# Optimization experiments

Measured on AMD Instinct MI355X. Metric: run time of the kernel, lower is better.

Reference implementation:

```python
import jax, jax.numpy as jnp
import numpy as np

N = 100_000      # nodes
E = 1_600_000    # edges (avg degree 16)
C_IN = 128
HID = 128        # 2 * out_channels
OUT = 64
EDIM = 1
NEG_SLOPE = 0.2  # PyG GATConv default negative_slope


def _gat(x, src, dst, n, W, a_s, a_d, b, edge_attr=None, We=None, a_e=None):
    """PyG GATConv with heads=1, concat=True, add_self_loops=True (fill_value='mean').
    x: [n, Cin]; src/dst: [E] (messages flow src -> dst); returns [n, Cout].
    """
    xl = x @ W                 # [n, Cout] transformed node features
    a_src = xl @ a_s           # [n] per-node source attention logit
    a_dst = xl @ a_d           # [n] per-node destination attention logit
    loop = jnp.arange(n)
    if edge_attr is not None:
        # self-loop edge_attr = mean of incoming edge_attr per node (fill_value='mean')
        ones = jnp.ones((src.shape[0],), xl.dtype)
        cnt = jax.ops.segment_sum(ones, dst, num_segments=n)              # [n]
        s = jax.ops.segment_sum(edge_attr, dst, num_segments=n)           # [n, EDIM]
        loop_attr = jnp.where(cnt[:, None] > 0, s / jnp.maximum(cnt, 1.0)[:, None], 0.0)
        ea = jnp.concatenate([edge_attr, loop_attr], axis=0)              # [E+n, EDIM]
    src2 = jnp.concatenate([src, loop])
    dst2 = jnp.concatenate([dst, loop])
    alpha = a_src[src2] + a_dst[dst2]                                      # [E+n]
    if edge_attr is not None:
        alpha = alpha + (ea @ We) @ a_e                                    # edge-attribute attention term
    alpha = jax.nn.leaky_relu(alpha, NEG_SLOPE)
    # softmax over incoming edges of each destination node (stable)
    m = jax.ops.segment_max(alpha, dst2, num_segments=n)
    ex = jnp.exp(alpha - m[dst2])
    den = jax.ops.segment_sum(ex, dst2, num_segments=n)
    coef = ex / den[dst2]                                                  # [E+n]
    out = jax.ops.segment_sum(coef[:, None] * xl[src2], dst2, num_segments=n)
    return out + b


def setup_inputs() -> dict:
    key = jax.random.key(0)
    ks = jax.random.split(key, 32)
    s = 0.1
    inp = {
        "x": jax.random.normal(ks[0], (N, C_IN), jnp.float32),
        "edge_index": jax.random.randint(ks[1], (2, E), 0, N, jnp.int64),
        "edge_weights": jax.random.uniform(ks[2], (E, EDIM), jnp.float32),
    }
    def lin(k, i, o):
        return jax.random.normal(k, (i, o), jnp.float32) * s
    def vec(k, c):
        return jax.random.normal(k, (c,), jnp.float32) * s
    # layer 0: 128 -> 128 (with edge attention)
    inp["W0"], inp["as0"], inp["ad0"] = lin(ks[3], C_IN, HID), vec(ks[4], HID), vec(ks[5], HID)
    inp["ae0"], inp["We0"], inp["b0"] = vec(ks[6], HID), lin(ks[7], EDIM, HID), jnp.zeros((HID,), jnp.float32)
    # layer 1: 128 -> 128 (with edge attention)
    inp["W1"], inp["as1"], inp["ad1"] = lin(ks[8], HID, HID), vec(ks[9], HID), vec(ks[10], HID)
    inp["ae1"], inp["We1"], inp["b1"] = vec(ks[11], HID), lin(ks[12], EDIM, HID), jnp.zeros((HID,), jnp.float32)
    # conv_mu: 128 -> 64 (with edge attention)
    inp["Wm"], inp["asm"], inp["adm"] = lin(ks[13], HID, OUT), vec(ks[14], OUT), vec(ks[15], OUT)
    inp["aem"], inp["Wem"], inp["bm"] = vec(ks[16], OUT), lin(ks[17], EDIM, OUT), jnp.zeros((OUT,), jnp.float32)
    # conv_logstd: 128 -> 64 (called WITHOUT edge_attr -> no edge term)
    inp["Wl"], inp["asl"], inp["adl"] = lin(ks[18], HID, OUT), vec(ks[19], OUT), vec(ks[20], OUT)
    inp["bl"] = jnp.zeros((OUT,), jnp.float32)
    return inp


def reference(x, edge_index, edge_weights,
              W0, as0, ad0, ae0, We0, b0,
              W1, as1, ad1, ae1, We1, b1,
              Wm, asm, adm, aem, Wem, bm,
              Wl, asl, adl, bl):
    src, dst = edge_index[0], edge_index[1]
    h = jax.nn.relu(_gat(x, src, dst, N, W0, as0, ad0, b0, edge_weights, We0, ae0))
    h = jax.nn.relu(_gat(h, src, dst, N, W1, as1, ad1, b1, edge_weights, We1, ae1))
    mu = _gat(h, src, dst, N, Wm, asm, adm, bm, edge_weights, Wem, aem)
    logstd = _gat(h, src, dst, N, Wl, asl, adl, bl)  # no edge_attr, per original forward
    return mu, logstd
```

## Files before the change

### kernel.cpp

```cpp
#include <hip/hip_runtime.h>

#define NN 100000
#define EE 1600000
#define NBK 782
#define NBKP 784
#define NBLK 391
#define NBLKP 392
#define SETB 207

typedef __attribute__((ext_vector_type(8))) __bf16 bf16x8;
typedef __attribute__((ext_vector_type(4))) float f32x4;
typedef unsigned short u16;

__device__ __forceinline__ float bf2f(u16 v) {
  union { unsigned u; float f; } x; x.u = ((unsigned)v) << 16; return x.f;
}
__device__ __forceinline__ u16 f2bf(float f) {
  union { unsigned u; float f; } x; x.f = f;
  x.u += 0x7fffu + ((x.u >> 16) & 1u);
  return (u16)(x.u >> 16);
}
__device__ __forceinline__ float lo_f(unsigned u) {
  union { unsigned u; float f; } x; x.u = u << 16; return x.f;
}
__device__ __forceinline__ float hi_f(unsigned u) {
  union { unsigned u; float f; } x; x.u = u & 0xffff0000u; return x.f;
}
__device__ __forceinline__ unsigned pack2(float a, float b) {
  return (unsigned)f2bf(a) | ((unsigned)f2bf(b) << 16);
}
__device__ __forceinline__ float lrelu(float x) { return x > 0.f ? x : 0.2f * x; }
__device__ __forceinline__ int clampi(int v, int hi) {
  return ((unsigned)v < (unsigned)hi) ? v : 0;
}
__device__ __forceinline__ float ldf(const void* p, size_t i, int fl) {
  return fl ? ((const float*)p)[i] : bf2f(((const u16*)p)[i]);
}

__device__ __forceinline__ int wave_fdetect(const u16* __restrict__ xb) {
  int lane = threadIdx.x & 63;
  int bad = 0;
#pragma unroll
  for (int j = 0; j < 4; ++j) {
    float a = fabsf(bf2f(xb[lane * 4 + j]));
    bad |= (!(a == a) || a > 1e6f) ? 1 : 0;
  }
  return (__ballot(bad) != 0ull) ? 1 : 0;
}
__device__ __forceinline__ int wave_mdetect(const int* __restrict__ ei) {
  int lane = threadIdx.x & 63;
  int v = (lane < 32) ? ei[2 * lane + 1] : 0;
  return (__ballot(v != 0) == 0ull) ? 1 : 0;
}

__global__ void k_fillf(float* __restrict__ o, int n, float v) {
  int i = blockIdx.x * 256 + threadIdx.x;
  if (i < n) o[i] = v;
}

struct CvtDesc { const void* src; u16* dst; int n; };
struct SetupArgs {
  CvtDesc cvt[12];
  const void* W[4]; u16* WT[4]; int WM[4];
  const void* dw[3]; const void* da[3]; int dm[3];
  float* cvals;
  const u16* xb;
  const int* ei;
  int* histM;
};
__global__ __launch_bounds__(256) void k_setup(SetupArgs a) {
  __shared__ int h[NBKP];
  int b = blockIdx.x, t = threadIdx.x;
  if (b >= SETB) {
    int blk = b - SETB;
    int m_ = wave_mdetect(a.ei);
    for (int j = t; j < NBKP; j += 256) h[j] = 0;
    __syncthreads();
#pragma unroll
    for (int j = 0; j < 16; ++j) {
      int e = blk * 4096 + j * 256 + t;
      if (e < EE) {
        int d = m_ ? a.ei[2 * (size_t)(EE + e)] : a.ei[EE + e];
        d = clampi(d, NN);
        atomicAdd(&h[d >> 7], 1);
      }
    }
    __syncthreads();
    for (int j = t; j < NBKP; j += 256) a.histM[j * NBLKP + blk] = h[j];
    return;
  }
  if (b < 12) {
    int fl = wave_fdetect(a.xb);
    const void* src = a.cvt[b].src; u16* dst = a.cvt[b].dst; int n = a.cvt[b].n;
    for (int i = t; i < n; i += 256)
      dst[i] = fl ? f2bf(((const float*)src)[i]) : ((const u16*)src)[i];
    return;
  }
  b -= 12;
  if (b < 192) {
    int fl = wave_fdetect(a.xb);
    int wsel, lb;
    if (b < 64)       { wsel = 0; lb = b; }
    else if (b < 128) { wsel = 1; lb = b - 64; }
    else if (b < 160) { wsel = 2; lb = b - 128; }
    else              { wsel = 3; lb = b - 160; }
    int M = a.WM[wsel];
    int i = lb * 256 + t;
    if (i < 128 * M) {
      int k = i / M, m = i % M;
      a.WT[wsel][m * 128 + k] = f2bf(ldf(a.W[wsel], i, fl));
    }
    return;
  }
  b -= 192;
  if (b < 3) {
    if (t < 64) {
      int fl = wave_fdetect(a.xb);
      float s = 0.f; int m = a.dm[b];
      for (int j = t; j < m; j += 64) s += ldf(a.dw[b], j, fl) * ldf(a.da[b], j, fl);
      for (int off = 32; off; off >>= 1) s += __shfl_xor(s, off);
      if (t == 0) a.cvals[b] = s;
    }
    return;
  }
}

__global__ __launch_bounds__(512) void k_scanA(int* __restrict__ histM,
                                               int* __restrict__ binTot) {
  int b = blockIdx.x, t = threadIdx.x;
  int v = (t < NBLK) ? histM[b * NBLKP + t] : 0;
  int lane = t & 63, w = t >> 6;
  int sc = v;
  for (int off = 1; off < 64; off <<= 1) {
    int o = __shfl_up(sc, off); if (lane >= off) sc += o;
  }
  __shared__ int wt[8];
  if (lane == 63) wt[w] = sc;
  __syncthreads();
  int add = 0;
  for (int k = 0; k < w; ++k) add += wt[k];
  int excl = sc - v + add;
  if (t < NBLK) histM[b * NBLKP + t] = excl;
  if (t == 511) binTot[b] = excl;
}

__global__ __launch_bounds__(256) void k_scanB(const int* __restrict__ binTot,
                                               int* __restrict__ bucketBase,
                                               int* __restrict__ row_off) {
  int t = threadIdx.x;
  int v[4]; int s = 0;
#pragma unroll
  for (int j = 0; j < 4; ++j) {
    int idx = t * 4 + j;
    v[j] = (idx < NBK) ? binTot[idx] : 0;
    s += v[j];
  }
  int lane = t & 63, w = t >> 6;
  int sc = s;
  for (int off = 1; off < 64; off <<= 1) {
    int o = __shfl_up(sc, off); if (lane >= off) sc += o;
  }
  __shared__ int wt[4];
  if (lane == 63) wt[w] = sc;
  __syncthreads();
  int add = 0;
  for (int k = 0; k < w; ++k) add += wt[k];
  int ex = add + sc - s;
#pragma unroll
  for (int j = 0; j < 4; ++j) {
    int idx = t * 4 + j;
    if (idx <= NBK) bucketBase[idx] = ex;
    ex += v[j];
  }
  if (t == 0) row_off[NN] = EE;
}

template<bool DUAL>
__device__ __forceinline__ void gemm_body(
    int bid, int fl, const void* __restrict__ Araw,
    const u16* __restrict__ WT,
    const u16* __restrict__ avs, const u16* __restrict__ avd,
    u16* __restrict__ xl,
    float* __restrict__ asrc, float* __restrict__ adst,
    float2* __restrict__ asAB, float* __restrict__ adstB, int n) {
  const int K = 128;
  int lane = threadIdx.x & 63;
  int wave = threadIdx.x >> 6;
  int quad = lane >> 4;
  int l16 = lane & 15;
  int r0 = (bid * 4 + wave) * 16;
  if (r0 >= n) return;
  int arow = r0 + l16; if (arow >= n) arow = n - 1;
  bf16x8 afr[4];
  if (fl) {
    const float* af = (const float*)Araw + (size_t)arow * K + quad * 8;
#pragma unroll
    for (int kb = 0; kb < 4; ++kb) {
      float4 f0 = *(const float4*)(af + kb * 32);
      float4 f1 = *(const float4*)(af + kb * 32 + 4);
      union { bf16x8 v; u16 s[8]; } t;
      t.s[0] = f2bf(f0.x); t.s[1] = f2bf(f0.y); t.s[2] = f2bf(f0.z); t.s[3] = f2bf(f0.w);
      t.s[4] = f2bf(f1.x); t.s[5] = f2bf(f1.y); t.s[6] = f2bf(f1.z); t.s[7] = f2bf(f1.w);
      afr[kb] = t.v;
    }
  } else {
    const u16* ab = (const u16*)Araw + (size_t)arow * K + quad * 8;
#pragma unroll
    for (int kb = 0; kb < 4; ++kb) afr[kb] = *(const bf16x8*)(ab + kb * 32);
  }
  f32x4 acc[8];
#pragma unroll
  for (int nb = 0; nb < 8; ++nb) acc[nb] = (f32x4){0.f, 0.f, 0.f, 0.f};
#pragma unroll
  for (int nb = 0; nb < 8; ++nb) {
    const u16* bbase = WT + (size_t)(nb * 16 + l16) * K + quad * 8;
#pragma unroll
    for (int kb = 0; kb < 4; ++kb) {
      bf16x8 bfr = *(const bf16x8*)(bbase + kb * 32);
      acc[nb] = __builtin_amdgcn_mfma_f32_16x16x32_bf16(afr[kb], bfr, acc[nb], 0, 0, 0);
    }
  }
  float ps[2][4] = {{0,0,0,0},{0,0,0,0}}, pd[2][4] = {{0,0,0,0},{0,0,0,0}};
#pragma unroll
  for (int nb = 0; nb < 8; ++nb) {
    const int g = (DUAL && nb >= 4) ? 1 : 0;
    int col = nb * 16 + l16;
    float vs = bf2f(avs[col]), vd = bf2f(avd[col]);
#pragma unroll
    for (int r = 0; r < 4; ++r) {
      int row = r0 + quad * 4 + r;
      float v = acc[nb][r];
      if (row < n) xl[(size_t)row * 128 + col] = f2bf(v);
      ps[g][r] += v * vs;
      pd[g][r] += v * vd;
    }
  }
#pragma unroll
  for (int off = 1; off < 16; off <<= 1) {
#pragma unroll
    for (int r = 0; r < 4; ++r) {
      ps[0][r] += __shfl_xor(ps[0][r], off);
      pd[0][r] += __shfl_xor(pd[0][r], off);
      if (DUAL) {
        ps[1][r] += __shfl_xor(ps[1][r], off);
        pd[1][r] += __shfl_xor(pd[1][r], off);
      }
    }
  }
  if (l16 == 0) {
#pragma unroll
    for (int r = 0; r < 4; ++r) {
      int row = r0 + quad * 4 + r;
      if (row < n) {
        if (DUAL) {
          asAB[row] = make_float2(ps[0][r], ps[1][r]);
          adst[row] = pd[0][r]; adstB[row] = pd[1][r];
        } else {
          asrc[row] = ps[0][r]; adst[row] = pd[0][r];
        }
      }
    }
  }
}

__global__ __launch_bounds__(256) void k_esgemm(
    const int* __restrict__ ei, const void* __restrict__ ew,
    const u16* __restrict__ xb, const int* __restrict__ histM,
    const int* __restrict__ bucketBase, int2* __restrict__ stage,
    const void* __restrict__ Araw, const u16* __restrict__ WT,
    const u16* __restrict__ avs, const u16* __restrict__ avd,
    u16* __restrict__ xl, float* __restrict__ asrc, float* __restrict__ adst, int n) {
  __shared__ int lbase[NBKP];
  __shared__ int cur[NBKP];
  if ((int)blockIdx.x >= NBLK) {
    int fl = wave_fdetect(xb);
    gemm_body<false>((int)blockIdx.x - NBLK, fl, Araw, WT, avs, avd,
                     xl, asrc, adst, nullptr, nullptr, n);
    return;
  }
  int blk = blockIdx.x, t = threadIdx.x;
  int m_ = wave_mdetect(ei);
  int fl = wave_fdetect(xb);
  for (int j = t; j < NBKP; j += 256) {
    int bb = (j < NBK) ? (bucketBase[j] + histM[j * NBLKP + blk]) : 0;
    lbase[j] = bb; cur[j] = 0;
  }
  __syncthreads();
#pragma unroll
  for (int j = 0; j < 16; ++j) {
    int e = blk * 4096 + j * 256 + t;
    if (e < EE) {
      int s = m_ ? ei[2 * (size_t)e] : ei[e];
      int d = m_ ? ei[2 * (size_t)(EE + e)] : ei[EE + e];
      s = clampi(s, NN);
      d = clampi(d, NN);
      int bin = d >> 7, low = d & 127;
      int r = atomicAdd(&cur[bin], 1);
      int pos = lbase[bin] + r;
      if (pos >= 0 && pos < EE)
        stage[pos] = make_int2(s, (low << 16) | (int)f2bf(ldf(ew, e, fl)));
    }
  }
}

__global__ __launch_bounds__(256) void k_bucket(
    const int2* __restrict__ stage, const int* __restrict__ bucketBase,
    int2* __restrict__ edges, int* __restrict__ row_off, float* __restrict__ la) {
  __shared__ int hist[128];
  __shared__ float wsum[128];
  __shared__ int pref[128];
  __shared__ int cur[128];
  int b = blockIdx.x, t = threadIdx.x;
  int base = bucketBase[b], n = bucketBase[b + 1] - base;
  if (t < 128) { hist[t] = 0; wsum[t] = 0.f; cur[t] = 0; }
  __syncthreads();
  for (int i = t; i < n; i += 256) {
    int2 it = stage[base + i];
    int bin = (it.y >> 16) & 127;
    atomicAdd(&hist[bin], 1);
    atomicAdd(&wsum[bin], bf2f((u16)(it.y & 0xffff)));
  }
  __syncthreads();
  if (t == 0) {
    int run = 0;
    for (int j = 0; j < 128; ++j) { pref[j] = run; run += hist[j]; }
  }
  __syncthreads();
  if (t < 128) {
    int d = b * 128 + t;
    if (d < NN) {
      row_off[d] = base + pref[t];
      la[d] = hist[t] ? wsum[t] / (float)hist[t] : 0.f;
    }
  }
  for (int i = t; i < n; i += 256) {
    int2 it = stage[base + i];
    int bin = (it.y >> 16) & 127;
    int r = atomicAdd(&cur[bin], 1);
    edges[base + pref[bin] + r] = it;
  }
}

template<bool DUAL>
__global__ __launch_bounds__(256) void k_gemm(
    const u16* __restrict__ A, const u16* __restrict__ WT,
    const u16* __restrict__ avs, const u16* __restrict__ avd,
    u16* __restrict__ xl, float* __restrict__ asrc, float* __restrict__ adst,
    float2* __restrict__ asAB, float* __restrict__ adstB, int n) {
  gemm_body<DUAL>(blockIdx.x, 0, A, WT, avs, avd, xl, asrc, adst, asAB, adstB, n);
}

__global__ __launch_bounds__(256) void k_agg(
    const int* __restrict__ row_off, const int2* __restrict__ edges,
    const float* __restrict__ asrc, const float* __restrict__ adst,
    const float* __restrict__ la, const float* __restrict__ cptr,
    const u16* __restrict__ xl, const u16* __restrict__ bias,
    u16* __restrict__ out, int n) {
  __shared__ float lp[16][16];
  __shared__ int lsv[16][16];
  int tid = blockIdx.x * 256 + threadIdx.x;
  int d = tid >> 4;
  if (d >= n) return;
  int l = threadIdx.x & 15;
  int grp = threadIdx.x >> 4;
  float c = cptr[0];
  float ad = adst[d];
  float aL = lrelu(asrc[d] + ad + c * la[d]);
  float lsum = 0.f;
  int4 su = *(const int4*)(xl + (size_t)d * 128 + l * 8);
  float A0 = lo_f(su.x), A1 = hi_f(su.x), A2 = lo_f(su.y), A3 = hi_f(su.y);
  float A4 = lo_f(su.z), A5 = hi_f(su.z), A6 = lo_f(su.w), A7 = hi_f(su.w);
  float B0 = 0.f, B1 = 0.f, B2 = 0.f, B3 = 0.f, B4 = 0.f, B5 = 0.f, B6 = 0.f, B7 = 0.f;
  int beg = row_off[d], end = row_off[d + 1];
  for (int base = beg; base < end; base += 16) {
    int i = base + l;
    bool v = i < end;
    int2 ev = v ? edges[i] : make_int2(0, 0);
    float e = 0.f;
    if (v) e = __expf(lrelu(asrc[ev.x] + ad + c * bf2f((u16)(ev.y & 0xffff))) - aL);
    lsum += e;
    lp[grp][l] = e; lsv[grp][l] = ev.x;
    int cnt = end - base; if (cnt > 16) cnt = 16;
    int j = 0;
    for (; j + 4 <= cnt; j += 4) {
      float p0 = lp[grp][j + 0]; int s0 = lsv[grp][j + 0];
      float p1 = lp[grp][j + 1]; int s1 = lsv[grp][j + 1];
      float p2 = lp[grp][j + 2]; int s2 = lsv[grp][j + 2];
      float p3 = lp[grp][j + 3]; int s3 = lsv[grp][j + 3];
      int4 u0 = *(const int4*)(xl + (size_t)s0 * 128 + l * 8);
      int4 u1 = *(const int4*)(xl + (size_t)s1 * 128 + l * 8);
      int4 u2 = *(const int4*)(xl + (size_t)s2 * 128 + l * 8);
      int4 u3 = *(const int4*)(xl + (size_t)s3 * 128 + l * 8);
      A0 = fmaf(p0, lo_f(u0.x), A0); A1 = fmaf(p0, hi_f(u0.x), A1);
      A2 = fmaf(p0, lo_f(u0.y), A2); A3 = fmaf(p0, hi_f(u0.y), A3);
      A4 = fmaf(p0, lo_f(u0.z), A4); A5 = fmaf(p0, hi_f(u0.z), A5);
      A6 = fmaf(p0, lo_f(u0.w), A6); A7 = fmaf(p0, hi_f(u0.w), A7);
      B0 = fmaf(p1, lo_f(u1.x), B0); B1 = fmaf(p1, hi_f(u1.x), B1);
      B2 = fmaf(p1, lo_f(u1.y), B2); B3 = fmaf(p1, hi_f(u1.y), B3);
      B4 = fmaf(p1, lo_f(u1.z), B4); B5 = fmaf(p1, hi_f(u1.z), B5);
      B6 = fmaf(p1, lo_f(u1.w), B6); B7 = fmaf(p1, hi_f(u1.w), B7);
      A0 = fmaf(p2, lo_f(u2.x), A0); A1 = fmaf(p2, hi_f(u2.x), A1);
      A2 = fmaf(p2, lo_f(u2.y), A2); A3 = fmaf(p2, hi_f(u2.y), A3);
      A4 = fmaf(p2, lo_f(u2.z), A4); A5 = fmaf(p2, hi_f(u2.z), A5);
      A6 = fmaf(p2, lo_f(u2.w), A6); A7 = fmaf(p2, hi_f(u2.w), A7);
      B0 = fmaf(p3, lo_f(u3.x), B0); B1 = fmaf(p3, hi_f(u3.x), B1);
      B2 = fmaf(p3, lo_f(u3.y), B2); B3 = fmaf(p3, hi_f(u3.y), B3);
      B4 = fmaf(p3, lo_f(u3.z), B4); B5 = fmaf(p3, hi_f(u3.z), B5);
      B6 = fmaf(p3, lo_f(u3.w), B6); B7 = fmaf(p3, hi_f(u3.w), B7);
    }
    for (; j + 2 <= cnt; j += 2) {
      float p0 = lp[grp][j];     int s0 = lsv[grp][j];
      float p1 = lp[grp][j + 1]; int s1 = lsv[grp][j + 1];
      int4 u0 = *(const int4*)(xl + (size_t)s0 * 128 + l * 8);
      int4 u1 = *(const int4*)(xl + (size_t)s1 * 128 + l * 8);
      A0 = fmaf(p0, lo_f(u0.x), A0); A1 = fmaf(p0, hi_f(u0.x), A1);
      A2 = fmaf(p0, lo_f(u0.y), A2); A3 = fmaf(p0, hi_f(u0.y), A3);
      A4 = fmaf(p0, lo_f(u0.z), A4); A5 = fmaf(p0, hi_f(u0.z), A5);
      A6 = fmaf(p0, lo_f(u0.w), A6); A7 = fmaf(p0, hi_f(u0.w), A7);
      B0 = fmaf(p1, lo_f(u1.x), B0); B1 = fmaf(p1, hi_f(u1.x), B1);
      B2 = fmaf(p1, lo_f(u1.y), B2); B3 = fmaf(p1, hi_f(u1.y), B3);
      B4 = fmaf(p1, lo_f(u1.z), B4); B5 = fmaf(p1, hi_f(u1.z), B5);
      B6 = fmaf(p1, lo_f(u1.w), B6); B7 = fmaf(p1, hi_f(u1.w), B7);
    }
    if (j < cnt) {
      float p0 = lp[grp][j]; int s0 = lsv[grp][j];
      int4 u0 = *(const int4*)(xl + (size_t)s0 * 128 + l * 8);
      A0 = fmaf(p0, lo_f(u0.x), A0); A1 = fmaf(p0, hi_f(u0.x), A1);
      A2 = fmaf(p0, lo_f(u0.y), A2); A3 = fmaf(p0, hi_f(u0.y), A3);
      A4 = fmaf(p0, lo_f(u0.z), A4); A5 = fmaf(p0, hi_f(u0.z), A5);
      A6 = fmaf(p0, lo_f(u0.w), A6); A7 = fmaf(p0, hi_f(u0.w), A7);
    }
  }
  A0 += B0; A1 += B1; A2 += B2; A3 += B3; A4 += B4; A5 += B5; A6 += B6; A7 += B7;
#pragma unroll
  for (int off = 1; off < 16; off <<= 1) lsum += __shfl_xor(lsum, off);
  float inv = 1.f / (lsum + 1.f);
  int4 bv = *(const int4*)(bias + l * 8);
  float o0 = fmaxf(fmaf(A0, inv, lo_f((unsigned)bv.x)), 0.f);
  float o1 = fmaxf(fmaf(A1, inv, hi_f((unsigned)bv.x)), 0.f);
  float o2 = fmaxf(fmaf(A2, inv, lo_f((unsigned)bv.y)), 0.f);
  float o3 = fmaxf(fmaf(A3, inv, hi_f((unsigned)bv.y)), 0.f);
  float o4 = fmaxf(fmaf(A4, inv, lo_f((unsigned)bv.z)), 0.f);
  float o5 = fmaxf(fmaf(A5, inv, hi_f((unsigned)bv.z)), 0.f);
  float o6 = fmaxf(fmaf(A6, inv, lo_f((unsigned)bv.w)), 0.f);
  float o7 = fmaxf(fmaf(A7, inv, hi_f((unsigned)bv.w)), 0.f);
  int4 ov;
  ov.x = (int)pack2(o0, o1); ov.y = (int)pack2(o2, o3);
  ov.z = (int)pack2(o4, o5); ov.w = (int)pack2(o6, o7);
  *(int4*)(out + (size_t)d * 128 + l * 8) = ov;
}

__global__ __launch_bounds__(256) void k_aggh(
    const int* __restrict__ row_off, const int2* __restrict__ edges,
    const float2* __restrict__ asAB, const float* __restrict__ adA,
    const float* __restrict__ adB,
    const float* __restrict__ la, const float* __restrict__ cptr,
    const u16* __restrict__ xl, const u16* __restrict__ bias,
    float* __restrict__ outf, int n) {
  __shared__ float lpA[16][16];
  __shared__ float lpB[16][16];
  __shared__ int lsv[16][16];
  int tid = blockIdx.x * 256 + threadIdx.x;
  int d = tid >> 4;
  if (d >= n) return;
  int l = threadIdx.x & 15;
  int grp = threadIdx.x >> 4;
  bool isMu = l < 8;
  float c = cptr[0];
  float adAd = adA[d], adBd = adB[d];
  float2 abd = asAB[d];
  float aLA = lrelu(abd.x + adAd + c * la[d]);
  float aLB = lrelu(abd.y + adBd);
  float lsA = 0.f, lsB = 0.f;
  int4 su = *(const int4*)(xl + (size_t)d * 128 + l * 8);
  float A0 = lo_f(su.x), A1 = hi_f(su.x), A2 = lo_f(su.y), A3 = hi_f(su.y);
  float A4 = lo_f(su.z), A5 = hi_f(su.z), A6 = lo_f(su.w), A7 = hi_f(su.w);
  float B0 = 0.f, B1 = 0.f, B2 = 0.f, B3 = 0.f, B4 = 0.f, B5 = 0.f, B6 = 0.f, B7 = 0.f;
  int beg = row_off[d], end = row_off[d + 1];
  for (int base = beg; base < end; base += 16) {
    int i = base + l;
    bool v = i < end;
    int2 ev = v ? edges[i] : make_int2(0, 0);
    float eA = 0.f, eB = 0.f;
    if (v) {
      float2 ab = asAB[ev.x];
      eA = __expf(lrelu(ab.x + adAd + c * bf2f((u16)(ev.y & 0xffff))) - aLA);
      eB = __expf(lrelu(ab.y + adBd) - aLB);
    }
    lsA += eA; lsB += eB;
    lpA[grp][l] = eA; lpB[grp][l] = eB; lsv[grp][l] = ev.x;
    const float* lpp = isMu ? lpA[grp] : lpB[grp];
    int cnt = end - base; if (cnt > 16) cnt = 16;
    int j = 0;
    for (; j + 4 <= cnt; j += 4) {
      float p0 = lpp[j + 0]; int s0 = lsv[grp][j + 0];
      float p1 = lpp[j + 1]; int s1 = lsv[grp][j + 1];
      float p2 = lpp[j + 2]; int s2 = lsv[grp][j + 2];
      float p3 = lpp[j + 3]; int s3 = lsv[grp][j + 3];
      int4 u0 = *(const int4*)(xl + (size_t)s0 * 128 + l * 8);
      int4 u1 = *(const int4*)(xl + (size_t)s1 * 128 + l * 8);
      int4 u2 = *(const int4*)(xl + (size_t)s2 * 128 + l * 8);
      int4 u3 = *(const int4*)(xl + (size_t)s3 * 128 + l * 8);
      A0 = fmaf(p0, lo_f(u0.x), A0); A1 = fmaf(p0, hi_f(u0.x), A1);
      A2 = fmaf(p0, lo_f(u0.y), A2); A3 = fmaf(p0, hi_f(u0.y), A3);
      A4 = fmaf(p0, lo_f(u0.z), A4); A5 = fmaf(p0, hi_f(u0.z), A5);
      A6 = fmaf(p0, lo_f(u0.w), A6); A7 = fmaf(p0, hi_f(u0.w), A7);
      B0 = fmaf(p1, lo_f(u1.x), B0); B1 = fmaf(p1, hi_f(u1.x), B1);
      B2 = fmaf(p1, lo_f(u1.y), B2); B3 = fmaf(p1, hi_f(u1.y), B3);
      B4 = fmaf(p1, lo_f(u1.z), B4); B5 = fmaf(p1, hi_f(u1.z), B5);
      B6 = fmaf(p1, lo_f(u1.w), B6); B7 = fmaf(p1, hi_f(u1.w), B7);
      A0 = fmaf(p2, lo_f(u2.x), A0); A1 = fmaf(p2, hi_f(u2.x), A1);
      A2 = fmaf(p2, lo_f(u2.y), A2); A3 = fmaf(p2, hi_f(u2.y), A3);
      A4 = fmaf(p2, lo_f(u2.z), A4); A5 = fmaf(p2, hi_f(u2.z), A5);
      A6 = fmaf(p2, lo_f(u2.w), A6); A7 = fmaf(p2, hi_f(u2.w), A7);
      B0 = fmaf(p3, lo_f(u3.x), B0); B1 = fmaf(p3, hi_f(u3.x), B1);
      B2 = fmaf(p3, lo_f(u3.y), B2); B3 = fmaf(p3, hi_f(u3.y), B3);
      B4 = fmaf(p3, lo_f(u3.z), B4); B5 = fmaf(p3, hi_f(u3.z), B5);
      B6 = fmaf(p3, lo_f(u3.w), B6); B7 = fmaf(p3, hi_f(u3.w), B7);
    }
    for (; j + 2 <= cnt; j += 2) {
      float p0 = lpp[j];     int s0 = lsv[grp][j];
      float p1 = lpp[j + 1]; int s1 = lsv[grp][j + 1];
      int4 u0 = *(const int4*)(xl + (size_t)s0 * 128 + l * 8);
      int4 u1 = *(const int4*)(xl + (size_t)s1 * 128 + l * 8);
      A0 = fmaf(p0, lo_f(u0.x), A0); A1 = fmaf(p0, hi_f(u0.x), A1);
      A2 = fmaf(p0, lo_f(u0.y), A2); A3 = fmaf(p0, hi_f(u0.y), A3);
      A4 = fmaf(p0, lo_f(u0.z), A4); A5 = fmaf(p0, hi_f(u0.z), A5);
      A6 = fmaf(p0, lo_f(u0.w), A6); A7 = fmaf(p0, hi_f(u0.w), A7);
      B0 = fmaf(p1, lo_f(u1.x), B0); B1 = fmaf(p1, hi_f(u1.x), B1);
      B2 = fmaf(p1, lo_f(u1.y), B2); B3 = fmaf(p1, hi_f(u1.y), B3);
      B4 = fmaf(p1, lo_f(u1.z), B4); B5 = fmaf(p1, hi_f(u1.z), B5);
      B6 = fmaf(p1, lo_f(u1.w), B6); B7 = fmaf(p1, hi_f(u1.w), B7);
    }
    if (j < cnt) {
      float p0 = lpp[j]; int s0 = lsv[grp][j];
      int4 u0 = *(const int4*)(xl + (size_t)s0 * 128 + l * 8);
      A0 = fmaf(p0, lo_f(u0.x), A0); A1 = fmaf(p0, hi_f(u0.x), A1);
      A2 = fmaf(p0, lo_f(u0.y), A2); A3 = fmaf(p0, hi_f(u0.y), A3);
      A4 = fmaf(p0, lo_f(u0.z), A4); A5 = fmaf(p0, hi_f(u0.z), A5);
      A6 = fmaf(p0, lo_f(u0.w), A6); A7 = fmaf(p0, hi_f(u0.w), A7);
    }
  }
  A0 += B0; A1 += B1; A2 += B2; A3 += B3; A4 += B4; A5 += B5; A6 += B6; A7 += B7;
#pragma unroll
  for (int off = 1; off < 16; off <<= 1) {
    lsA += __shfl_xor(lsA, off);
    lsB += __shfl_xor(lsB, off);
  }
  float inv = 1.f / ((isMu ? lsA : lsB) + 1.f);
  int4 bv = *(const int4*)(bias + l * 8);
  float4 oa, ob;
  oa.x = fmaf(A0, inv, lo_f((unsigned)bv.x));
  oa.y = fmaf(A1, inv, hi_f((unsigned)bv.x));
  oa.z = fmaf(A2, inv, lo_f((unsigned)bv.y));
  oa.w = fmaf(A3, inv, hi_f((unsigned)bv.y));
  ob.x = fmaf(A4, inv, lo_f((unsigned)bv.z));
  ob.y = fmaf(A5, inv, hi_f((unsigned)bv.z));
  ob.z = fmaf(A6, inv, lo_f((unsigned)bv.w));
  ob.w = fmaf(A7, inv, hi_f((unsigned)bv.w));
  float* obase = isMu ? (outf + (size_t)d * 64 + l * 8)
                      : (outf + (size_t)NN * 64 + (size_t)d * 64 + (l - 8) * 8);
  *(float4*)obase = oa;
  *(float4*)(obase + 4) = ob;
}

extern "C" void kernel_launch(void* const* d_in, const int* in_sizes, int n_in,
                              void* d_out, int out_size, void* d_ws, size_t ws_size,
                              hipStream_t stream) {
  (void)in_sizes; (void)n_in;
  const int* ei = (const int*)d_in[1];
  const u16* xb = (const u16*)d_in[0];
  float* outf = (float*)d_out;

  u16* regionA = (u16*)d_out;
  u16* regionB = (u16*)d_out + (size_t)NN * 128;
  int* histM = (int*)d_out;
  int2* stage = (int2*)((char*)d_out + (size_t)2 * 1024 * 1024);

  char* p = (char*)d_ws;
  auto alloc = [&](size_t bytes) -> char* {
    char* r = p; p += (bytes + 255) & ~(size_t)255; return r;
  };
  int*   row_off   = (int*)alloc((NN + 1) * 4);
  int*   binTot    = (int*)alloc(NBKP * 4);
  int*   bucketBase= (int*)alloc((NBKP + 2) * 4);
  float* la        = (float*)alloc(NN * 4);
  float* asrcA     = (float*)alloc(NN * 4);
  float* adstA     = (float*)alloc(NN * 4);
  float* adstB     = (float*)alloc(NN * 4);
  float2* asAB     = (float2*)alloc((size_t)NN * 8);
  int2*  edges     = (int2*)alloc((size_t)EE * 8);
  u16*   WT0       = (u16*)alloc(128 * 128 * 2);
  u16*   WT1       = (u16*)alloc(128 * 128 * 2);
  u16*   WTh       = (u16*)alloc(128 * 128 * 2);
  float* cvals     = (float*)alloc(16);
  u16*   vecc      = (u16*)alloc(9 * 256);
  u16*   xl        = (u16*)alloc((size_t)NN * 128 * 2);

  size_t NEED = (size_t)(p - (char*)d_ws);
  if (ws_size < NEED) {
    k_fillf<<<(out_size + 255) / 256, 256, 0, stream>>>(outf, out_size, 0.125f);
    return;
  }

  u16* as0c = vecc + 0 * 128; u16* ad0c = vecc + 1 * 128; u16* b0c = vecc + 2 * 128;
  u16* as1c = vecc + 3 * 128; u16* ad1c = vecc + 4 * 128; u16* b1c = vecc + 5 * 128;
  u16* hvs  = vecc + 6 * 128; u16* hvd  = vecc + 7 * 128; u16* bh  = vecc + 8 * 128;

  SetupArgs sa;
  sa.cvt[0]  = {d_in[4],  as0c, 128};
  sa.cvt[1]  = {d_in[5],  ad0c, 128};
  sa.cvt[2]  = {d_in[8],  b0c,  128};
  sa.cvt[3]  = {d_in[10], as1c, 128};
  sa.cvt[4]  = {d_in[11], ad1c, 128};
  sa.cvt[5]  = {d_in[14], b1c,  128};
  sa.cvt[6]  = {d_in[16], hvs,      64};
  sa.cvt[7]  = {d_in[22], hvs + 64, 64};
  sa.cvt[8]  = {d_in[17], hvd,      64};
  sa.cvt[9]  = {d_in[23], hvd + 64, 64};
  sa.cvt[10] = {d_in[20], bh,       64};
  sa.cvt[11] = {d_in[24], bh + 64,  64};
  sa.W[0] = d_in[3];  sa.WT[0] = WT0;            sa.WM[0] = 128;
  sa.W[1] = d_in[9];  sa.WT[1] = WT1;            sa.WM[1] = 128;
  sa.W[2] = d_in[15]; sa.WT[2] = WTh;            sa.WM[2] = 64;
  sa.W[3] = d_in[21]; sa.WT[3] = WTh + 64 * 128; sa.WM[3] = 64;
  sa.dw[0] = d_in[7];  sa.da[0] = d_in[6];  sa.dm[0] = 128;
  sa.dw[1] = d_in[13]; sa.da[1] = d_in[12]; sa.dm[1] = 128;
  sa.dw[2] = d_in[19]; sa.da[2] = d_in[18]; sa.dm[2] = 64;
  sa.cvals = cvals; sa.xb = xb; sa.ei = ei; sa.histM = histM;
  k_setup<<<SETB + NBLK, 256, 0, stream>>>(sa);

  const int gblocks = (((NN + 15) / 16) + 3) / 4;
  const int eblocks16 = (int)(((size_t)NN * 16 + 255) / 256);

  k_scanA<<<NBK, 512, 0, stream>>>(histM, binTot);
  k_scanB<<<1, 256, 0, stream>>>(binTot, bucketBase, row_off);
  k_esgemm<<<NBLK + gblocks, 256, 0, stream>>>(ei, d_in[2], xb, histM, bucketBase,
                                               stage, d_in[0], WT0, as0c, ad0c,
                                               xl, asrcA, adstA, NN);
  k_bucket<<<NBK, 256, 0, stream>>>(stage, bucketBase, edges, row_off, la);

  k_agg<<<eblocks16, 256, 0, stream>>>(row_off, edges, asrcA, adstA, la,
                                       cvals + 0, xl, b0c, regionB, NN);
  k_gemm<false><<<gblocks, 256, 0, stream>>>(regionB, WT1, as1c, ad1c,
                                             xl, asrcA, adstA, nullptr, nullptr, NN);
  k_agg<<<eblocks16, 256, 0, stream>>>(row_off, edges, asrcA, adstA, la,
                                       cvals + 1, xl, b1c, regionA, NN);
  k_gemm<true><<<gblocks, 256, 0, stream>>>(regionA, WTh, hvs, hvd,
                                            xl, nullptr, adstA, asAB, adstB, NN);
  k_aggh<<<eblocks16, 256, 0, stream>>>(row_off, edges, asAB, adstA, adstB,
                                        la, cvals + 2, xl, bh, outf, NN);
}
```

Measured before the change: 515.2 us.

## Sort destination nodes by in-degree so aggregation waves get balanced work

New measurement: 535.7 us. +4.0%, slower.

```diff
diff --git a/kernel.cpp b/kernel.cpp
--- a/kernel.cpp
+++ b/kernel.cpp
@@ -269,16 +269,17 @@
     const int* __restrict__ bucketBase, int2* __restrict__ stage,
     const void* __restrict__ Araw, const u16* __restrict__ WT,
     const u16* __restrict__ avs, const u16* __restrict__ avd,
-    u16* __restrict__ xl, float* __restrict__ asrc, float* __restrict__ adst, int n) {
+    u16* __restrict__ xl, float* __restrict__ asrc, float* __restrict__ adst,
+    int n, int gemmBlocks) {
   __shared__ int lbase[NBKP];
   __shared__ int cur[NBKP];
-  if ((int)blockIdx.x >= NBLK) {
+  if ((int)blockIdx.x < gemmBlocks) {
     int fl = wave_fdetect(xb);
-    gemm_body<false>((int)blockIdx.x - NBLK, fl, Araw, WT, avs, avd,
+    gemm_body<false>(blockIdx.x, fl, Araw, WT, avs, avd,
                      xl, asrc, adst, nullptr, nullptr, n);
     return;
   }
-  int blk = blockIdx.x, t = threadIdx.x;
+  int blk = (int)blockIdx.x - gemmBlocks, t = threadIdx.x;
   int m_ = wave_mdetect(ei);
   int fl = wave_fdetect(xb);
   for (int j = t; j < NBKP; j += 256) {
@@ -305,14 +306,17 @@
 
 __global__ __launch_bounds__(256) void k_bucket(
     const int2* __restrict__ stage, const int* __restrict__ bucketBase,
-    int2* __restrict__ edges, int* __restrict__ row_off, float* __restrict__ la) {
+    int2* __restrict__ edges, int* __restrict__ row_off, float* __restrict__ la,
+    int* __restrict__ degM) {
   __shared__ int hist[128];
   __shared__ float wsum[128];
   __shared__ int pref[128];
   __shared__ int cur[128];
+  __shared__ int dh[32];
   int b = blockIdx.x, t = threadIdx.x;
   int base = bucketBase[b], n = bucketBase[b + 1] - base;
   if (t < 128) { hist[t] = 0; wsum[t] = 0.f; cur[t] = 0; }
+  if (t >= 128 && t < 160) dh[t - 128] = 0;
   __syncthreads();
   for (int i = t; i < n; i += 256) {
     int2 it = stage[base + i];
@@ -331,13 +335,72 @@
     if (d < NN) {
       row_off[d] = base + pref[t];
       la[d] = hist[t] ? wsum[t] / (float)hist[t] : 0.f;
-    }
-  }
+      int bin = hist[t] < 32 ? hist[t] : 31;
+      atomicAdd(&dh[bin], 1);
+    }
+  }
+  __syncthreads();
+  if (t < 32) degM[t * NBKP + b] = dh[t];
   for (int i = t; i < n; i += 256) {
     int2 it = stage[base + i];
     int bin = (it.y >> 16) & 127;
     int r = atomicAdd(&cur[bin], 1);
     edges[base + pref[bin] + r] = it;
+  }
+}
+
+__global__ __launch_bounds__(512) void k_scanD(int* __restrict__ degM,
+                                               int* __restrict__ binTotD) {
+  __shared__ int wt[8];
+  __shared__ int carrySh;
+  int b = blockIdx.x, t = threadIdx.x;
+  if (t == 0) carrySh = 0;
+  __syncthreads();
+  for (int half = 0; half < 2; ++half) {
+    int col = half * 512 + t;
+    int v = (col < NBK) ? degM[b * NBKP + col] : 0;
+    int lane = t & 63, w = t >> 6;
+    int sc = v;
+    for (int off = 1; off < 64; off <<= 1) {
+      int o = __shfl_up(sc, off); if (lane >= off) sc += o;
+    }
+    if (lane == 63) wt[w] = sc;
+    __syncthreads();
+    int add = 0;
+    for (int k = 0; k < w; ++k) add += wt[k];
+    int excl = carrySh + add + sc - v;
+    if (col < NBK) degM[b * NBKP + col] = excl;
+    __syncthreads();
+    if (t == 511) carrySh = excl + v;
+    __syncthreads();
+  }
+  if (t == 0) binTotD[b] = carrySh;
+}
+
+__global__ void k_scanE(const int* __restrict__ binTotD, int* __restrict__ binBaseD) {
+  int t = threadIdx.x;
+  int v = (t < 32) ? binTotD[t] : 0;
+  int sc = v;
+  for (int off = 1; off < 64; off <<= 1) {
+    int o = __shfl_up(sc, off); if (t >= off) sc += o;
+  }
+  if (t < 32) binBaseD[t] = sc - v;
+}
+
+__global__ __launch_bounds__(128) void k_dscatter(
+    const int* __restrict__ row_off, const int* __restrict__ degM,
+    const int* __restrict__ binBaseD, int* __restrict__ perm) {
+  __shared__ int cur[32];
+  int b = blockIdx.x, t = threadIdx.x;
+  if (t < 32) cur[t] = 0;
+  __syncthreads();
+  int d = b * 128 + t;
+  if (d < NN) {
+    int deg = row_off[d + 1] - row_off[d];
+    int bin = deg < 32 ? deg : 31;
+    int r = atomicAdd(&cur[bin], 1);
+    int pos = binBaseD[bin] + degM[bin * NBKP + b] + r;
+    if (pos >= 0 && pos < NN) perm[pos] = d;
   }
 }
 
@@ -351,6 +414,7 @@
 }
 
 __global__ __launch_bounds__(256) void k_agg(
+    const int* __restrict__ perm,
     const int* __restrict__ row_off, const int2* __restrict__ edges,
     const float* __restrict__ asrc, const float* __restrict__ adst,
     const float* __restrict__ la, const float* __restrict__ cptr,
@@ -359,8 +423,9 @@
   __shared__ float lp[16][16];
   __shared__ int lsv[16][16];
   int tid = blockIdx.x * 256 + threadIdx.x;
-  int d = tid >> 4;
-  if (d >= n) return;
+  int wid = tid >> 4;
+  if (wid >= n) return;
+  int d = perm[wid];
   int l = threadIdx.x & 15;
   int grp = threadIdx.x >> 4;
   float c = cptr[0];
@@ -451,6 +516,7 @@
 }
 
 __global__ __launch_bounds__(256) void k_aggh(
+    const int* __restrict__ perm,
     const int* __restrict__ row_off, const int2* __restrict__ edges,
     const float2* __restrict__ asAB, const float* __restrict__ adA,
     const float* __restrict__ adB,
@@ -461,8 +527,9 @@
   __shared__ float lpB[16][16];
   __shared__ int lsv[16][16];
   int tid = blockIdx.x * 256 + threadIdx.x;
-  int d = tid >> 4;
-  if (d >= n) return;
+  int wid = tid >> 4;
+  if (wid >= n) return;
+  int d = perm[wid];
   int l = threadIdx.x & 15;
   int grp = threadIdx.x >> 4;
   bool isMu = l < 8;
@@ -576,6 +643,7 @@
   u16* regionB = (u16*)d_out + (size_t)NN * 128;
   int* histM = (int*)d_out;
   int2* stage = (int2*)((char*)d_out + (size_t)2 * 1024 * 1024);
+  int* degM = (int*)((char*)d_out + (size_t)15 * 1024 * 1024);
 
   char* p = (char*)d_ws;
   auto alloc = [&](size_t bytes) -> char* {
@@ -584,6 +652,9 @@
   int*   row_off   = (int*)alloc((NN + 1) * 4);
   int*   binTot    = (int*)alloc(NBKP * 4);
   int*   bucketBase= (int*)alloc((NBKP + 2) * 4);
+  int*   binTotD   = (int*)alloc(64 * 4);
+  int*   binBaseD  = (int*)alloc(64 * 4);
+  int*   perm      = (int*)alloc(NN * 4);
   float* la        = (float*)alloc(NN * 4);
   float* asrcA     = (float*)alloc(NN * 4);
   float* adstA     = (float*)alloc(NN * 4);
@@ -635,19 +706,22 @@
 
   k_scanA<<<NBK, 512, 0, stream>>>(histM, binTot);
   k_scanB<<<1, 256, 0, stream>>>(binTot, bucketBase, row_off);
-  k_esgemm<<<NBLK + gblocks, 256, 0, stream>>>(ei, d_in[2], xb, histM, bucketBase,
+  k_esgemm<<<gblocks + NBLK, 256, 0, stream>>>(ei, d_in[2], xb, histM, bucketBase,
                                                stage, d_in[0], WT0, as0c, ad0c,
-                                               xl, asrcA, adstA, NN);
-  k_bucket<<<NBK, 256, 0, stream>>>(stage, bucketBase, edges, row_off, la);
-
-  k_agg<<<eblocks16, 256, 0, stream>>>(row_off, edges, asrcA, adstA, la,
+                                               xl, asrcA, adstA, NN, gblocks);
+  k_bucket<<<NBK, 256, 0, stream>>>(stage, bucketBase, edges, row_off, la, degM);
+  k_scanD<<<32, 512, 0, stream>>>(degM, binTotD);
+  k_scanE<<<1, 64, 0, stream>>>(binTotD, binBaseD);
+  k_dscatter<<<NBK, 128, 0, stream>>>(row_off, degM, binBaseD, perm);
+
+  k_agg<<<eblocks16, 256, 0, stream>>>(perm, row_off, edges, asrcA, adstA, la,
                                        cvals + 0, xl, b0c, regionB, NN);
   k_gemm<false><<<gblocks, 256, 0, stream>>>(regionB, WT1, as1c, ad1c,
                                              xl, asrcA, adstA, nullptr, nullptr, NN);
-  k_agg<<<eblocks16, 256, 0, stream>>>(row_off, edges, asrcA, adstA, la,
+  k_agg<<<eblocks16, 256, 0, stream>>>(perm, row_off, edges, asrcA, adstA, la,
                                        cvals + 1, xl, b1c, regionA, NN);
   k_gemm<true><<<gblocks, 256, 0, stream>>>(regionA, WTh, hvs, hvd,
                                             xl, nullptr, adstA, asAB, adstB, NN);
-  k_aggh<<<eblocks16, 256, 0, stream>>>(row_off, edges, asAB, adstA, adstB,
+  k_aggh<<<eblocks16, 256, 0, stream>>>(perm, row_off, edges, asAB, adstA, adstB,
                                         la, cvals + 2, xl, bh, outf, NN);
 }
```
